# Optimization experiments

Hardware: AMD Instinct MI355X
Metric: run time of the kernel (lower is better)

## Reference

```python
import jax, jax.numpy as jnp
import numpy as np
from math import sqrt

D_MODEL = 768
N_HEADS = 12
D_K = 64
D_V = 64
LN_EPS = 1e-5
NEG = -1e9


def layer_norm(x, g, b):
    mu = jnp.mean(x, axis=-1, keepdims=True)
    var = jnp.mean((x - mu) ** 2, axis=-1, keepdims=True)
    return (x - mu) * jax.lax.rsqrt(var + LN_EPS) * g + b


def setup_inputs() -> dict:
    key = jax.random.key(0)
    ks = jax.random.split(key, 8)
    B, S = 4, 1024
    pro1 = jax.random.normal(ks[0], (B, S, D_MODEL), dtype=jnp.float32)
    pro2 = jax.random.normal(ks[1], (B, S, D_MODEL), dtype=jnp.float32)
    # attn_mask is [B, H, S2, S1]; transpose(2,3) masks scores [B,H,S1,S2]
    mask1_2 = jax.random.bernoulli(ks[2], 0.3, (B, N_HEADS, S, S))
    sc = 1.0 / np.sqrt(D_MODEL)
    W_Q = jax.random.normal(ks[3], (D_MODEL, D_K * N_HEADS), dtype=jnp.float32) * sc
    W_K = jax.random.normal(ks[4], (D_MODEL, D_K * N_HEADS), dtype=jnp.float32) * sc
    fc1 = jax.random.normal(ks[5], (D_V * N_HEADS, D_MODEL), dtype=jnp.float32) * sc
    g1 = jnp.ones((D_MODEL,), jnp.float32)
    b1 = jnp.zeros((D_MODEL,), jnp.float32)
    g2 = jnp.ones((D_MODEL,), jnp.float32)
    b2 = jnp.zeros((D_MODEL,), jnp.float32)
    return {"pro1": pro1, "pro2": pro2, "mask1_2": mask1_2,
            "W_Q": W_Q, "W_K": W_K, "fc1": fc1,
            "g1": g1, "b1": b1, "g2": g2, "b2": b2}


def reference(pro1, pro2, mask1_2, W_Q, W_K, fc1, g1, b1, g2, b2):
    B, S1, _ = pro1.shape
    S2 = pro2.shape[1]
    # project and split heads: [B, H, S, d_k]
    Q = (pro1 @ W_Q).reshape(B, S1, N_HEADS, D_K).transpose(0, 2, 1, 3)
    K = (pro2 @ W_K).reshape(B, S2, N_HEADS, D_K).transpose(0, 2, 1, 3)
    scores = jnp.einsum('bhsd,bhtd->bhst', Q, K) / sqrt(D_K)  # [B,H,S1,S2]
    mask = jnp.swapaxes(mask1_2, 2, 3)  # attn_mask.transpose(2,3)
    scores = jnp.where(mask, NEG, scores)
    attn1 = jax.nn.softmax(scores, axis=-1)                  # over S2
    attn2 = jax.nn.softmax(jnp.swapaxes(scores, -1, -2), axis=-1)  # over S1
    ctx1 = jnp.einsum('bhst,bhtd->bhsd', attn1, K)  # [B,H,S1,d_k]
    ctx2 = jnp.einsum('bhts,bhsd->bhtd', attn2, Q)  # [B,H,S2,d_k]
    c1 = ctx1.transpose(0, 2, 1, 3).reshape(B, S1, N_HEADS * D_V)
    c2 = ctx2.transpose(0, 2, 1, 3).reshape(B, S2, N_HEADS * D_V)
    # NOTE: original applies fc1 to BOTH branches (fc2 is dead code)
    o1 = layer_norm(c1 @ fc1, g1, b1)
    o2 = layer_norm(c2 @ fc1, g2, b2)
    return (o1, o2)
```

## Files before the change

### kernel.cpp

```cpp
#include <hip/hip_runtime.h>
#include <hip/hip_bf16.h>
#include <stdint.h>

#define S 1024
#define DMODEL 768
#define NH 12
#define DK 64
#define BB 4
#define BH 48
#define M4 4096
#define NEGV -1e9f

typedef __attribute__((ext_vector_type(8))) short bf16x8;
typedef __attribute__((ext_vector_type(4))) float f32x4;

static __device__ __forceinline__ unsigned short f2bf(float f) {
  unsigned int u = __float_as_uint(f);
  unsigned int r = u + 0x7FFFu + ((u >> 16) & 1u);
  return (unsigned short)(r >> 16);
}
static __device__ __forceinline__ float bf2f(unsigned short h) {
  return __uint_as_float(((unsigned int)h) << 16);
}
static __device__ __forceinline__ bf16x8 ldfrag(const unsigned short* p) {
  uint4 q = *reinterpret_cast<const uint4*>(p);
  return __builtin_bit_cast(bf16x8, q);
}

__global__ __launch_bounds__(256) void k_convert(const float* __restrict__ in,
                                                 unsigned short* __restrict__ out, int n4) {
  int i = blockIdx.x * 256 + threadIdx.x;
  if (i < n4) {
    float4 v = reinterpret_cast<const float4*>(in)[i];
    ushort4 o;
    o.x = f2bf(v.x); o.y = f2bf(v.y); o.z = f2bf(v.z); o.w = f2bf(v.w);
    reinterpret_cast<ushort4*>(out)[i] = o;
  }
}

__global__ __launch_bounds__(256) void k_transpose(const float* w0, const float* w1, const float* w2,
                                                   unsigned short* o0, unsigned short* o1, unsigned short* o2) {
  const float* in = blockIdx.z == 0 ? w0 : (blockIdx.z == 1 ? w1 : w2);
  unsigned short* out = blockIdx.z == 0 ? o0 : (blockIdx.z == 1 ? o1 : o2);
  __shared__ float tile[32][33];
  int n0 = blockIdx.x * 32, k0 = blockIdx.y * 32;
  int tid = threadIdx.x;
  int r = tid >> 3, c = (tid & 7) * 4;
  float4 v = *reinterpret_cast<const float4*>(in + (size_t)(k0 + r) * DMODEL + n0 + c);
  tile[r][c] = v.x; tile[r][c + 1] = v.y; tile[r][c + 2] = v.z; tile[r][c + 3] = v.w;
  __syncthreads();
  ushort4 o;
  o.x = f2bf(tile[c + 0][r]);
  o.y = f2bf(tile[c + 1][r]);
  o.z = f2bf(tile[c + 2][r]);
  o.w = f2bf(tile[c + 3][r]);
  *reinterpret_cast<ushort4*>(out + (size_t)(n0 + r) * DMODEL + k0 + c) = o;
}

__global__ __launch_bounds__(256) void k_pack(const int* __restrict__ mask,
                                              unsigned int* __restrict__ mp1,
                                              unsigned int* __restrict__ mp2) {
  int bh = blockIdx.y;
  int w = threadIdx.x >> 6, lane = threadIdx.x & 63;
  int tile = blockIdx.x * 4 + w;
  int ti = tile >> 4, tj = tile & 15;
  int t0 = ti * 64, s0 = tj * 64;
  const int* mb = mask + (size_t)bh * S * S;
  unsigned long long rowword = 0;
#pragma unroll 8
  for (int r = 0; r < 64; ++r) {
    int v = mb[(size_t)(t0 + r) * S + s0 + lane];
    unsigned long long b = __ballot(v != 0);
    if (lane == r) rowword = b;
  }
  unsigned int* p2 = mp2 + (size_t)bh * 32 * S;
  p2[((s0 >> 5) + 0) * S + t0 + lane] = (unsigned int)rowword;
  p2[((s0 >> 5) + 1) * S + t0 + lane] = (unsigned int)(rowword >> 32);
  unsigned long long colword = 0;
#pragma unroll
  for (int s = 0; s < 64; ++s) {
    unsigned long long b = __ballot((rowword >> s) & 1ull);
    if (lane == s) colword = b;
  }
  unsigned int* p1 = mp1 + (size_t)bh * 32 * S;
  p1[((t0 >> 5) + 0) * S + s0 + lane] = (unsigned int)colword;
  p1[((t0 >> 5) + 1) * S + s0 + lane] = (unsigned int)(colword >> 32);
}

__global__ __launch_bounds__(256) void k_gemm128(
    int mode,
    const unsigned short* __restrict__ A0, const unsigned short* __restrict__ A1,
    const unsigned short* __restrict__ Bt0, const unsigned short* __restrict__ Bt1,
    unsigned short* __restrict__ oQ0, unsigned short* __restrict__ oQ1,
    unsigned short* __restrict__ oT0, unsigned short* __restrict__ oT1,
    float* __restrict__ oF0, float* __restrict__ oF1) {
  const unsigned short* A = blockIdx.z ? A1 : A0;
  const unsigned short* Bt = blockIdx.z ? Bt1 : Bt0;
  __shared__ __align__(16) unsigned short As[128 * 72];
  __shared__ __align__(16) unsigned short Bs[128 * 72];
  int tid = threadIdx.x;
  int m0 = blockIdx.x * 128, n0 = blockIdx.y * 128;
  int w = tid >> 6, lane = tid & 63, lane15 = lane & 15, quad = lane >> 4;
  int row0 = (w >> 1) * 64, col0 = (w & 1) * 64;
  f32x4 acc[4][4] = {};
  int sr = tid >> 2, sc = (tid & 3) * 16;
  const unsigned short* gA0 = A + (size_t)(m0 + sr) * DMODEL + sc;
  const unsigned short* gA1 = A + (size_t)(m0 + 64 + sr) * DMODEL + sc;
  const unsigned short* gB0 = Bt + (size_t)(n0 + sr) * DMODEL + sc;
  const unsigned short* gB1 = Bt + (size_t)(n0 + 64 + sr) * DMODEL + sc;
  uint4 va0 = *reinterpret_cast<const uint4*>(gA0);
  uint4 va1 = *reinterpret_cast<const uint4*>(gA1);
  uint4 vb0 = *reinterpret_cast<const uint4*>(gB0);
  uint4 vb1 = *reinterpret_cast<const uint4*>(gB1);
  uint4 va0b = *reinterpret_cast<const uint4*>(gA0 + 8);
  uint4 va1b = *reinterpret_cast<const uint4*>(gA1 + 8);
  uint4 vb0b = *reinterpret_cast<const uint4*>(gB0 + 8);
  uint4 vb1b = *reinterpret_cast<const uint4*>(gB1 + 8);
  for (int kc = 0; kc < 12; ++kc) {
    __syncthreads();
    *reinterpret_cast<uint4*>(&As[sr * 72 + sc]) = va0;
    *reinterpret_cast<uint4*>(&As[sr * 72 + sc + 8]) = va0b;
    *reinterpret_cast<uint4*>(&As[(64 + sr) * 72 + sc]) = va1;
    *reinterpret_cast<uint4*>(&As[(64 + sr) * 72 + sc + 8]) = va1b;
    *reinterpret_cast<uint4*>(&Bs[sr * 72 + sc]) = vb0;
    *reinterpret_cast<uint4*>(&Bs[sr * 72 + sc + 8]) = vb0b;
    *reinterpret_cast<uint4*>(&Bs[(64 + sr) * 72 + sc]) = vb1;
    *reinterpret_cast<uint4*>(&Bs[(64 + sr) * 72 + sc + 8]) = vb1b;
    if (kc < 11) {
      int k0 = (kc + 1) * 64;
      va0 = *reinterpret_cast<const uint4*>(gA0 + k0);
      va1 = *reinterpret_cast<const uint4*>(gA1 + k0);
      vb0 = *reinterpret_cast<const uint4*>(gB0 + k0);
      vb1 = *reinterpret_cast<const uint4*>(gB1 + k0);
      va0b = *reinterpret_cast<const uint4*>(gA0 + k0 + 8);
      va1b = *reinterpret_cast<const uint4*>(gA1 + k0 + 8);
      vb0b = *reinterpret_cast<const uint4*>(gB0 + k0 + 8);
      vb1b = *reinterpret_cast<const uint4*>(gB1 + k0 + 8);
    }
    __syncthreads();
#pragma unroll
    for (int ks = 0; ks < 2; ++ks) {
      int kk = ks * 32 + quad * 8;
      bf16x8 a[4], b[4];
#pragma unroll
      for (int i = 0; i < 4; ++i) a[i] = ldfrag(&As[(row0 + i * 16 + lane15) * 72 + kk]);
#pragma unroll
      for (int j = 0; j < 4; ++j) b[j] = ldfrag(&Bs[(col0 + j * 16 + lane15) * 72 + kk]);
#pragma unroll
      for (int i = 0; i < 4; ++i)
#pragma unroll
        for (int j = 0; j < 4; ++j)
          acc[i][j] = __builtin_amdgcn_mfma_f32_16x16x32_bf16(a[i], b[j], acc[i][j], 0, 0, 0);
    }
  }
  if (mode == 0) {
    unsigned short* out = blockIdx.z ? oQ1 : oQ0;
    unsigned short* outT = blockIdx.z ? oT1 : oT0;
#pragma unroll
    for (int i = 0; i < 4; ++i)
#pragma unroll
      for (int j = 0; j < 4; ++j)
#pragma unroll
        for (int reg = 0; reg < 4; ++reg) {
          int m = m0 + row0 + i * 16 + quad * 4 + reg;
          int n = n0 + col0 + j * 16 + lane15;
          int b = m >> 10, s = m & 1023, h = n >> 6, d = n & 63;
          unsigned short bv = f2bf(acc[i][j][reg]);
          out[(((size_t)(b * NH + h)) * S + s) * DK + d] = bv;
          outT[(((size_t)(b * NH + h)) * DK + d) * S + s] = bv;
        }
  } else {
    float* out = blockIdx.z ? oF1 : oF0;
#pragma unroll
    for (int i = 0; i < 4; ++i)
#pragma unroll
      for (int j = 0; j < 4; ++j)
#pragma unroll
        for (int reg = 0; reg < 4; ++reg) {
          int m = m0 + row0 + i * 16 + quad * 4 + reg;
          int n = n0 + col0 + j * 16 + lane15;
          out[(size_t)m * DMODEL + n] = acc[i][j][reg];
        }
  }
}

__global__ __launch_bounds__(256, 4) void k_attn(
    const unsigned short* __restrict__ Qb, const unsigned short* __restrict__ Kb,
    const unsigned short* __restrict__ QT, const unsigned short* __restrict__ KT,
    const unsigned int* __restrict__ mp1, const unsigned int* __restrict__ mp2,
    unsigned short* __restrict__ c1, unsigned short* __restrict__ c2) {
  int bh = blockIdx.y, path = blockIdx.z;
  int s0b = blockIdx.x * 64;
  const unsigned short* X = path ? Kb : Qb;
  const unsigned short* Y = path ? Qb : Kb;
  const unsigned short* YT = path ? QT : KT;
  const unsigned int* mp = path ? mp2 : mp1;
  unsigned short* outc = path ? c2 : c1;

  __shared__ __align__(16) unsigned short YS[64 * 72];
  __shared__ __align__(16) unsigned short YTS[64 * 72];
  __shared__ __align__(16) unsigned short PS[4][16 * 72];
  __shared__ unsigned int MW[64 * 33];

  const unsigned short* Xb = X + (size_t)bh * S * DK;
  const unsigned short* Yb = Y + (size_t)bh * S * DK;
  const unsigned short* YTb = YT + (size_t)bh * DK * S;
  const unsigned int* mb = mp + (size_t)bh * 32 * S;

  int tid = threadIdx.x;
  int w = tid >> 6, lane = tid & 63, lane15 = lane & 15, quad = lane >> 4;
  int s0 = s0b + w * 16;

  {
    int wd = tid >> 3, r8 = (tid & 7) * 8;
    uint4 v0 = *reinterpret_cast<const uint4*>(mb + (size_t)wd * S + s0b + r8);
    uint4 v1 = *reinterpret_cast<const uint4*>(mb + (size_t)wd * S + s0b + r8 + 4);
    MW[(r8 + 0) * 33 + wd] = v0.x; MW[(r8 + 1) * 33 + wd] = v0.y;
    MW[(r8 + 2) * 33 + wd] = v0.z; MW[(r8 + 3) * 33 + wd] = v0.w;
    MW[(r8 + 4) * 33 + wd] = v1.x; MW[(r8 + 5) * 33 + wd] = v1.y;
    MW[(r8 + 6) * 33 + wd] = v1.z; MW[(r8 + 7) * 33 + wd] = v1.w;
  }

  bf16x8 af0 = ldfrag(Xb + (size_t)(s0 + lane15) * DK + quad * 8);
  bf16x8 af1 = ldfrag(Xb + (size_t)(s0 + lane15) * DK + 32 + quad * 8);

  int sr4 = tid >> 2, sc4 = (tid & 3) * 16;
  const unsigned short* gY = Yb + (size_t)sr4 * DK + sc4;
  const unsigned short* gYT = YTb + (size_t)sr4 * S + sc4;
  uint4 y0 = *reinterpret_cast<const uint4*>(gY);
  uint4 y1 = *reinterpret_cast<const uint4*>(gY + 8);
  uint4 t0 = *reinterpret_cast<const uint4*>(gYT);
  uint4 t1 = *reinterpret_cast<const uint4*>(gYT + 8);

  f32x4 outa[4] = {};
  float lsum[4] = {0.f, 0.f, 0.f, 0.f};
  unsigned short* PSw = PS[w];

  for (int jc = 0; jc < 16; ++jc) {
    __syncthreads();
    *reinterpret_cast<uint4*>(&YS[sr4 * 72 + sc4]) = y0;
    *reinterpret_cast<uint4*>(&YS[sr4 * 72 + sc4 + 8]) = y1;
    *reinterpret_cast<uint4*>(&YTS[sr4 * 72 + sc4]) = t0;
    *reinterpret_cast<uint4*>(&YTS[sr4 * 72 + sc4 + 8]) = t1;
    {
      int jn = (jc + 1 < 16) ? (jc + 1) * 64 : jc * 64;
      y0 = *reinterpret_cast<const uint4*>(gY + (size_t)jn * DK);
      y1 = *reinterpret_cast<const uint4*>(gY + (size_t)jn * DK + 8);
      t0 = *reinterpret_cast<const uint4*>(gYT + jn);
      t1 = *reinterpret_cast<const uint4*>(gYT + jn + 8);
    }
    __syncthreads();

    int j0 = jc * 64;
    f32x4 sc[4];
#pragma unroll
    for (int st = 0; st < 4; ++st) {
      bf16x8 b0 = ldfrag(&YS[(st * 16 + lane15) * 72 + quad * 8]);
      bf16x8 b1 = ldfrag(&YS[(st * 16 + lane15) * 72 + 32 + quad * 8]);
      f32x4 a = {};
      a = __builtin_amdgcn_mfma_f32_16x16x32_bf16(af0, b0, a, 0, 0, 0);
      a = __builtin_amdgcn_mfma_f32_16x16x32_bf16(af1, b1, a, 0, 0, 0);
      sc[st] = a;
    }
    int w0 = j0 >> 5;
    unsigned int mw0[4], mw1[4];
#pragma unroll
    for (int reg = 0; reg < 4; ++reg) {
      int r = w * 16 + quad * 4 + reg;
      mw0[reg] = MW[r * 33 + w0];
      mw1[reg] = MW[r * 33 + w0 + 1];
    }
#pragma unroll
    for (int st = 0; st < 4; ++st) {
      unsigned int sh = (unsigned)((st & 1) * 16 + lane15);
#pragma unroll
      for (int reg = 0; reg < 4; ++reg) {
        unsigned int wd = (st < 2) ? mw0[reg] : mw1[reg];
        float e = __expf(sc[st][reg] * 0.125f);
        float p = ((wd >> sh) & 1u) ? 0.f : e;
        lsum[reg] += p;
        PSw[(quad * 4 + reg) * 72 + st * 16 + lane15] = f2bf(p);
      }
    }
#pragma unroll
    for (int half = 0; half < 2; ++half) {
      bf16x8 pa = ldfrag(&PSw[lane15 * 72 + half * 32 + quad * 8]);
#pragma unroll
      for (int dt = 0; dt < 4; ++dt) {
        bf16x8 bb = ldfrag(&YTS[(dt * 16 + lane15) * 72 + half * 32 + quad * 8]);
        outa[dt] = __builtin_amdgcn_mfma_f32_16x16x32_bf16(pa, bb, outa[dt], 0, 0, 0);
      }
    }
  }

#pragma unroll
  for (int reg = 0; reg < 4; ++reg) {
#pragma unroll
    for (int m = 1; m < 16; m <<= 1) lsum[reg] += __shfl_xor(lsum[reg], m);
    lsum[reg] = 1.0f / lsum[reg];
  }
  int b = bh / NH, h = bh % NH;
#pragma unroll
  for (int dt = 0; dt < 4; ++dt)
#pragma unroll
    for (int reg = 0; reg < 4; ++reg) {
      float v = outa[dt][reg] * lsum[reg];
      size_t idx = ((size_t)(b * S) + s0 + quad * 4 + reg) * DMODEL + h * DK + dt * 16 + lane15;
      outc[idx] = f2bf(v);
    }
}

__global__ __launch_bounds__(256) void k_ln(const float* __restrict__ f1, const float* __restrict__ f2,
                                            const float* __restrict__ g1, const float* __restrict__ b1,
                                            const float* __restrict__ g2, const float* __restrict__ b2,
                                            float* __restrict__ out) {
  int rowg = blockIdx.x;
  int sel = rowg >> 12;
  int row = rowg & 4095;
  const float* in = sel ? f2 : f1;
  const float* g = sel ? g2 : g1;
  const float* be = sel ? b2 : b1;
  int tid = threadIdx.x;
  const float* p = in + (size_t)row * DMODEL;
  float x0 = p[tid], x1 = p[tid + 256], x2 = p[tid + 512];
  float s = x0 + x1 + x2;
  float ss = x0 * x0 + x1 * x1 + x2 * x2;
#pragma unroll
  for (int m = 1; m < 64; m <<= 1) { s += __shfl_xor(s, m); ss += __shfl_xor(ss, m); }
  __shared__ float ps[4], pss[4];
  int w = tid >> 6;
  if ((tid & 63) == 0) { ps[w] = s; pss[w] = ss; }
  __syncthreads();
  s = ps[0] + ps[1] + ps[2] + ps[3];
  ss = pss[0] + pss[1] + pss[2] + pss[3];
  float mu = s * (1.0f / 768.0f);
  float var = ss * (1.0f / 768.0f) - mu * mu;
  float rstd = rsqrtf(var + 1e-5f);
  float* o = out + ((size_t)sel * M4 + row) * DMODEL;
  o[tid] = (x0 - mu) * rstd * g[tid] + be[tid];
  o[tid + 256] = (x1 - mu) * rstd * g[tid + 256] + be[tid + 256];
  o[tid + 512] = (x2 - mu) * rstd * g[tid + 512] + be[tid + 512];
}

extern "C" void kernel_launch(void* const* d_in, const int* in_sizes, int n_in,
                              void* d_out, int out_size, void* d_ws, size_t ws_size,
                              hipStream_t stream) {
  const float* pro1 = (const float*)d_in[0];
  const float* pro2 = (const float*)d_in[1];
  const int* mask = (const int*)d_in[2];
  const float* WQ = (const float*)d_in[3];
  const float* WK = (const float*)d_in[4];
  const float* FC1 = (const float*)d_in[5];
  const float* g1 = (const float*)d_in[6];
  const float* b1 = (const float*)d_in[7];
  const float* g2 = (const float*)d_in[8];
  const float* b2 = (const float*)d_in[9];
  float* out = (float*)d_out;
  char* ws = (char*)d_ws;

  unsigned short* pro1b = (unsigned short*)(ws + 0);
  unsigned short* pro2b = (unsigned short*)(ws + 6291456);
  float* f1 = (float*)(ws + 0);
  unsigned short* wqt = (unsigned short*)(ws + 12582912);
  unsigned short* wkt = (unsigned short*)(ws + 13762560);
  unsigned short* fc1t = (unsigned short*)(ws + 14942208);
  unsigned short* Qb = (unsigned short*)(ws + 16121856);
  unsigned short* Kb = (unsigned short*)(ws + 22413312);
  unsigned short* QT = (unsigned short*)(ws + 28704768);
  unsigned short* KT = (unsigned short*)(ws + 34996224);
  unsigned int* mp1 = (unsigned int*)(ws + 41287680);
  unsigned int* mp2 = (unsigned int*)(ws + 47579136);
  float* f2 = (float*)(ws + 41287680);
  unsigned short* c1 = (unsigned short*)(ws + 53870592);
  unsigned short* c2 = (unsigned short*)(ws + 60162048);

  k_convert<<<3072, 256, 0, stream>>>(pro1, pro1b, 786432);
  k_convert<<<3072, 256, 0, stream>>>(pro2, pro2b, 786432);
  k_transpose<<<dim3(24, 24, 3), 256, 0, stream>>>(WQ, WK, FC1, wqt, wkt, fc1t);
  k_pack<<<dim3(64, BH), 256, 0, stream>>>(mask, mp1, mp2);
  k_gemm128<<<dim3(32, 6, 2), 256, 0, stream>>>(0, pro1b, pro2b, wqt, wkt, Qb, Kb, QT, KT, nullptr, nullptr);
  k_attn<<<dim3(16, BH, 2), 256, 0, stream>>>(Qb, Kb, QT, KT, mp1, mp2, c1, c2);
  k_gemm128<<<dim3(32, 6, 2), 256, 0, stream>>>(1, c1, c2, fc1t, fc1t, nullptr, nullptr, nullptr, nullptr, f1, f2);
  k_ln<<<8192, 256, 0, stream>>>(f1, f2, g1, b1, g2, b2, out);
}
```

Before: 442.4 us.

## Fuse input conversion into QK GEMM and keep attention probabilities in registers

The separate fp32-to-bf16 conversion kernels are removed; the projection GEMM now loads fp32 inputs and packs them to bf16 while staging into shared memory. The transposed Q/K copies are written as fp16 using an identity-matrix MFMA to transpose accumulator fragments. The attention kernel processes 128 rows per block (32 per wave). It transposes the probability fragments in registers with an identity fp16 MFMA instead of round-tripping through shared memory, and does the PV product with fp16 MFMAs. This removes the LDS traffic for P and two kernel launches, at the cost of more registers (occupancy hint lowered to 3), extra MFMA work for the transposes, and fp16 precision for P and the transposed operands.

```diff
diff --git a/kernel.cpp b/kernel.cpp
--- a/kernel.cpp
+++ b/kernel.cpp
@@ -9,33 +9,25 @@
 #define BB 4
 #define BH 48
 #define M4 4096
-#define NEGV -1e9f
 
 typedef __attribute__((ext_vector_type(8))) short bf16x8;
 typedef __attribute__((ext_vector_type(4))) float f32x4;
+typedef __attribute__((ext_vector_type(4))) _Float16 f16x4;
 
 static __device__ __forceinline__ unsigned short f2bf(float f) {
   unsigned int u = __float_as_uint(f);
   unsigned int r = u + 0x7FFFu + ((u >> 16) & 1u);
   return (unsigned short)(r >> 16);
 }
-static __device__ __forceinline__ float bf2f(unsigned short h) {
-  return __uint_as_float(((unsigned int)h) << 16);
+static __device__ __forceinline__ unsigned int pk2(float a, float b) {
+  return (unsigned int)f2bf(a) | ((unsigned int)f2bf(b) << 16);
 }
 static __device__ __forceinline__ bf16x8 ldfrag(const unsigned short* p) {
   uint4 q = *reinterpret_cast<const uint4*>(p);
   return __builtin_bit_cast(bf16x8, q);
 }
-
-__global__ __launch_bounds__(256) void k_convert(const float* __restrict__ in,
-                                                 unsigned short* __restrict__ out, int n4) {
-  int i = blockIdx.x * 256 + threadIdx.x;
-  if (i < n4) {
-    float4 v = reinterpret_cast<const float4*>(in)[i];
-    ushort4 o;
-    o.x = f2bf(v.x); o.y = f2bf(v.y); o.z = f2bf(v.z); o.w = f2bf(v.w);
-    reinterpret_cast<ushort4*>(out)[i] = o;
-  }
+static __device__ __forceinline__ unsigned short h2u(_Float16 h) {
+  return __builtin_bit_cast(unsigned short, h);
 }
 
 __global__ __launch_bounds__(256) void k_transpose(const float* w0, const float* w1, const float* w2,
@@ -87,14 +79,16 @@
   p1[((t0 >> 5) + 1) * S + s0 + lane] = (unsigned int)(colword >> 32);
 }
 
-__global__ __launch_bounds__(256) void k_gemm128(
+__global__ __launch_bounds__(256, 2) void k_gemm128(
     int mode,
-    const unsigned short* __restrict__ A0, const unsigned short* __restrict__ A1,
+    const float* __restrict__ Af0, const float* __restrict__ Af1,
+    const unsigned short* __restrict__ Ab0, const unsigned short* __restrict__ Ab1,
     const unsigned short* __restrict__ Bt0, const unsigned short* __restrict__ Bt1,
     unsigned short* __restrict__ oQ0, unsigned short* __restrict__ oQ1,
     unsigned short* __restrict__ oT0, unsigned short* __restrict__ oT1,
     float* __restrict__ oF0, float* __restrict__ oF1) {
-  const unsigned short* A = blockIdx.z ? A1 : A0;
+  const float* Af = blockIdx.z ? Af1 : Af0;
+  const unsigned short* Ab = blockIdx.z ? Ab1 : Ab0;
   const unsigned short* Bt = blockIdx.z ? Bt1 : Bt0;
   __shared__ __align__(16) unsigned short As[128 * 72];
   __shared__ __align__(16) unsigned short Bs[128 * 72];
@@ -104,38 +98,72 @@
   int row0 = (w >> 1) * 64, col0 = (w & 1) * 64;
   f32x4 acc[4][4] = {};
   int sr = tid >> 2, sc = (tid & 3) * 16;
-  const unsigned short* gA0 = A + (size_t)(m0 + sr) * DMODEL + sc;
-  const unsigned short* gA1 = A + (size_t)(m0 + 64 + sr) * DMODEL + sc;
   const unsigned short* gB0 = Bt + (size_t)(n0 + sr) * DMODEL + sc;
   const unsigned short* gB1 = Bt + (size_t)(n0 + 64 + sr) * DMODEL + sc;
-  uint4 va0 = *reinterpret_cast<const uint4*>(gA0);
-  uint4 va1 = *reinterpret_cast<const uint4*>(gA1);
-  uint4 vb0 = *reinterpret_cast<const uint4*>(gB0);
-  uint4 vb1 = *reinterpret_cast<const uint4*>(gB1);
-  uint4 va0b = *reinterpret_cast<const uint4*>(gA0 + 8);
-  uint4 va1b = *reinterpret_cast<const uint4*>(gA1 + 8);
-  uint4 vb0b = *reinterpret_cast<const uint4*>(gB0 + 8);
-  uint4 vb1b = *reinterpret_cast<const uint4*>(gB1 + 8);
+  uint4 vb[2][2];
+  vb[0][0] = *reinterpret_cast<const uint4*>(gB0);
+  vb[0][1] = *reinterpret_cast<const uint4*>(gB0 + 8);
+  vb[1][0] = *reinterpret_cast<const uint4*>(gB1);
+  vb[1][1] = *reinterpret_cast<const uint4*>(gB1 + 8);
+  const float* gAf0 = Af + (size_t)(m0 + sr) * DMODEL + sc;
+  const float* gAf1 = Af + (size_t)(m0 + 64 + sr) * DMODEL + sc;
+  const unsigned short* gAb0 = Ab + (size_t)(m0 + sr) * DMODEL + sc;
+  const unsigned short* gAb1 = Ab + (size_t)(m0 + 64 + sr) * DMODEL + sc;
+  float4 fa[2][4];
+  uint4 va[2][2];
+  if (mode == 0) {
+#pragma unroll
+    for (int g = 0; g < 4; ++g) fa[0][g] = *reinterpret_cast<const float4*>(gAf0 + g * 4);
+#pragma unroll
+    for (int g = 0; g < 4; ++g) fa[1][g] = *reinterpret_cast<const float4*>(gAf1 + g * 4);
+  } else {
+    va[0][0] = *reinterpret_cast<const uint4*>(gAb0);
+    va[0][1] = *reinterpret_cast<const uint4*>(gAb0 + 8);
+    va[1][0] = *reinterpret_cast<const uint4*>(gAb1);
+    va[1][1] = *reinterpret_cast<const uint4*>(gAb1 + 8);
+  }
   for (int kc = 0; kc < 12; ++kc) {
     __syncthreads();
-    *reinterpret_cast<uint4*>(&As[sr * 72 + sc]) = va0;
-    *reinterpret_cast<uint4*>(&As[sr * 72 + sc + 8]) = va0b;
-    *reinterpret_cast<uint4*>(&As[(64 + sr) * 72 + sc]) = va1;
-    *reinterpret_cast<uint4*>(&As[(64 + sr) * 72 + sc + 8]) = va1b;
-    *reinterpret_cast<uint4*>(&Bs[sr * 72 + sc]) = vb0;
-    *reinterpret_cast<uint4*>(&Bs[sr * 72 + sc + 8]) = vb0b;
-    *reinterpret_cast<uint4*>(&Bs[(64 + sr) * 72 + sc]) = vb1;
-    *reinterpret_cast<uint4*>(&Bs[(64 + sr) * 72 + sc + 8]) = vb1b;
+    if (mode == 0) {
+#pragma unroll
+      for (int h2 = 0; h2 < 2; ++h2) {
+        uint4 u0, u1;
+        u0.x = pk2(fa[h2][0].x, fa[h2][0].y); u0.y = pk2(fa[h2][0].z, fa[h2][0].w);
+        u0.z = pk2(fa[h2][1].x, fa[h2][1].y); u0.w = pk2(fa[h2][1].z, fa[h2][1].w);
+        u1.x = pk2(fa[h2][2].x, fa[h2][2].y); u1.y = pk2(fa[h2][2].z, fa[h2][2].w);
+        u1.z = pk2(fa[h2][3].x, fa[h2][3].y); u1.w = pk2(fa[h2][3].z, fa[h2][3].w);
+        *reinterpret_cast<uint4*>(&As[(h2 * 64 + sr) * 72 + sc]) = u0;
+        *reinterpret_cast<uint4*>(&As[(h2 * 64 + sr) * 72 + sc + 8]) = u1;
+      }
+    } else {
+#pragma unroll
+      for (int h2 = 0; h2 < 2; ++h2) {
+        *reinterpret_cast<uint4*>(&As[(h2 * 64 + sr) * 72 + sc]) = va[h2][0];
+        *reinterpret_cast<uint4*>(&As[(h2 * 64 + sr) * 72 + sc + 8]) = va[h2][1];
+      }
+    }
+#pragma unroll
+    for (int h2 = 0; h2 < 2; ++h2) {
+      *reinterpret_cast<uint4*>(&Bs[(h2 * 64 + sr) * 72 + sc]) = vb[h2][0];
+      *reinterpret_cast<uint4*>(&Bs[(h2 * 64 + sr) * 72 + sc + 8]) = vb[h2][1];
+    }
     if (kc < 11) {
       int k0 = (kc + 1) * 64;
-      va0 = *reinterpret_cast<const uint4*>(gA0 + k0);
-      va1 = *reinterpret_cast<const uint4*>(gA1 + k0);
-      vb0 = *reinterpret_cast<const uint4*>(gB0 + k0);
-      vb1 = *reinterpret_cast<const uint4*>(gB1 + k0);
-      va0b = *reinterpret_cast<const uint4*>(gA0 + k0 + 8);
-      va1b = *reinterpret_cast<const uint4*>(gA1 + k0 + 8);
-      vb0b = *reinterpret_cast<const uint4*>(gB0 + k0 + 8);
-      vb1b = *reinterpret_cast<const uint4*>(gB1 + k0 + 8);
+      if (mode == 0) {
+#pragma unroll
+        for (int g = 0; g < 4; ++g) fa[0][g] = *reinterpret_cast<const float4*>(gAf0 + k0 + g * 4);
+#pragma unroll
+        for (int g = 0; g < 4; ++g) fa[1][g] = *reinterpret_cast<const float4*>(gAf1 + k0 + g * 4);
+      } else {
+        va[0][0] = *reinterpret_cast<const uint4*>(gAb0 + k0);
+        va[0][1] = *reinterpret_cast<const uint4*>(gAb0 + k0 + 8);
+        va[1][0] = *reinterpret_cast<const uint4*>(gAb1 + k0);
+        va[1][1] = *reinterpret_cast<const uint4*>(gAb1 + k0 + 8);
+      }
+      vb[0][0] = *reinterpret_cast<const uint4*>(gB0 + k0);
+      vb[0][1] = *reinterpret_cast<const uint4*>(gB0 + k0 + 8);
+      vb[1][0] = *reinterpret_cast<const uint4*>(gB1 + k0);
+      vb[1][1] = *reinterpret_cast<const uint4*>(gB1 + k0 + 8);
     }
     __syncthreads();
 #pragma unroll
@@ -156,19 +184,33 @@
   if (mode == 0) {
     unsigned short* out = blockIdx.z ? oQ1 : oQ0;
     unsigned short* outT = blockIdx.z ? oT1 : oT0;
+    f16x4 iden;
+#pragma unroll
+    for (int i = 0; i < 4; ++i) iden[i] = (_Float16)((quad * 4 + i) == lane15 ? 1.0f : 0.0f);
+    f32x4 zero4 = {};
 #pragma unroll
     for (int i = 0; i < 4; ++i)
 #pragma unroll
-      for (int j = 0; j < 4; ++j)
+      for (int j = 0; j < 4; ++j) {
 #pragma unroll
         for (int reg = 0; reg < 4; ++reg) {
           int m = m0 + row0 + i * 16 + quad * 4 + reg;
           int n = n0 + col0 + j * 16 + lane15;
           int b = m >> 10, s = m & 1023, h = n >> 6, d = n & 63;
-          unsigned short bv = f2bf(acc[i][j][reg]);
-          out[(((size_t)(b * NH + h)) * S + s) * DK + d] = bv;
-          outT[(((size_t)(b * NH + h)) * DK + d) * S + s] = bv;
+          out[(((size_t)(b * NH + h)) * S + s) * DK + d] = f2bf(acc[i][j][reg]);
         }
+        f16x4 cf;
+#pragma unroll
+        for (int reg = 0; reg < 4; ++reg) cf[reg] = (_Float16)acc[i][j][reg];
+        f32x4 tq = __builtin_amdgcn_mfma_f32_16x16x16f16(cf, iden, zero4, 0, 0, 0);
+#pragma unroll
+        for (int reg = 0; reg < 4; ++reg) {
+          int n = n0 + col0 + j * 16 + quad * 4 + reg;
+          int m = m0 + row0 + i * 16 + lane15;
+          int b = m >> 10, s = m & 1023, h = n >> 6, d = n & 63;
+          outT[(((size_t)(b * NH + h)) * DK + d) * S + s] = h2u((_Float16)tq[reg]);
+        }
+      }
   } else {
     float* out = blockIdx.z ? oF1 : oF0;
 #pragma unroll
@@ -184,13 +226,13 @@
   }
 }
 
-__global__ __launch_bounds__(256, 4) void k_attn(
+__global__ __launch_bounds__(256, 3) void k_attn(
     const unsigned short* __restrict__ Qb, const unsigned short* __restrict__ Kb,
     const unsigned short* __restrict__ QT, const unsigned short* __restrict__ KT,
     const unsigned int* __restrict__ mp1, const unsigned int* __restrict__ mp2,
     unsigned short* __restrict__ c1, unsigned short* __restrict__ c2) {
   int bh = blockIdx.y, path = blockIdx.z;
-  int s0b = blockIdx.x * 64;
+  int s0b = blockIdx.x * 128;
   const unsigned short* X = path ? Kb : Qb;
   const unsigned short* Y = path ? Qb : Kb;
   const unsigned short* YT = path ? QT : KT;
@@ -199,8 +241,7 @@
 
   __shared__ __align__(16) unsigned short YS[64 * 72];
   __shared__ __align__(16) unsigned short YTS[64 * 72];
-  __shared__ __align__(16) unsigned short PS[4][16 * 72];
-  __shared__ unsigned int MW[64 * 33];
+  __shared__ unsigned int MW[128 * 33];
 
   const unsigned short* Xb = X + (size_t)bh * S * DK;
   const unsigned short* Yb = Y + (size_t)bh * S * DK;
@@ -209,20 +250,31 @@
 
   int tid = threadIdx.x;
   int w = tid >> 6, lane = tid & 63, lane15 = lane & 15, quad = lane >> 4;
-  int s0 = s0b + w * 16;
+  int s0w = s0b + w * 32;
 
   {
-    int wd = tid >> 3, r8 = (tid & 7) * 8;
-    uint4 v0 = *reinterpret_cast<const uint4*>(mb + (size_t)wd * S + s0b + r8);
-    uint4 v1 = *reinterpret_cast<const uint4*>(mb + (size_t)wd * S + s0b + r8 + 4);
-    MW[(r8 + 0) * 33 + wd] = v0.x; MW[(r8 + 1) * 33 + wd] = v0.y;
-    MW[(r8 + 2) * 33 + wd] = v0.z; MW[(r8 + 3) * 33 + wd] = v0.w;
-    MW[(r8 + 4) * 33 + wd] = v1.x; MW[(r8 + 5) * 33 + wd] = v1.y;
-    MW[(r8 + 6) * 33 + wd] = v1.z; MW[(r8 + 7) * 33 + wd] = v1.w;
-  }
-
-  bf16x8 af0 = ldfrag(Xb + (size_t)(s0 + lane15) * DK + quad * 8);
-  bf16x8 af1 = ldfrag(Xb + (size_t)(s0 + lane15) * DK + 32 + quad * 8);
+    int wd = tid >> 3, rb = (tid & 7) * 16;
+#pragma unroll
+    for (int u = 0; u < 4; ++u) {
+      uint4 v = *reinterpret_cast<const uint4*>(mb + (size_t)wd * S + s0b + rb + u * 4);
+      MW[(rb + u * 4 + 0) * 33 + wd] = v.x;
+      MW[(rb + u * 4 + 1) * 33 + wd] = v.y;
+      MW[(rb + u * 4 + 2) * 33 + wd] = v.z;
+      MW[(rb + u * 4 + 3) * 33 + wd] = v.w;
+    }
+  }
+
+  bf16x8 af[2][2];
+#pragma unroll
+  for (int rg = 0; rg < 2; ++rg) {
+    af[rg][0] = ldfrag(Xb + (size_t)(s0w + rg * 16 + lane15) * DK + quad * 8);
+    af[rg][1] = ldfrag(Xb + (size_t)(s0w + rg * 16 + lane15) * DK + 32 + quad * 8);
+  }
+
+  f16x4 iden;
+#pragma unroll
+  for (int i = 0; i < 4; ++i) iden[i] = (_Float16)((quad * 4 + i) == lane15 ? 1.0f : 0.0f);
+  f32x4 zero4 = {};
 
   int sr4 = tid >> 2, sc4 = (tid & 3) * 16;
   const unsigned short* gY = Yb + (size_t)sr4 * DK + sc4;
@@ -232,9 +284,8 @@
   uint4 t0 = *reinterpret_cast<const uint4*>(gYT);
   uint4 t1 = *reinterpret_cast<const uint4*>(gYT + 8);
 
-  f32x4 outa[4] = {};
-  float lsum[4] = {0.f, 0.f, 0.f, 0.f};
-  unsigned short* PSw = PS[w];
+  f32x4 outa[2][4] = {};
+  float lsum[2][4] = {};
 
   for (int jc = 0; jc < 16; ++jc) {
     __syncthreads();
@@ -252,62 +303,85 @@
     __syncthreads();
 
     int j0 = jc * 64;
-    f32x4 sc[4];
+    int w0 = j0 >> 5;
+    f32x4 sc[2][4];
 #pragma unroll
     for (int st = 0; st < 4; ++st) {
       bf16x8 b0 = ldfrag(&YS[(st * 16 + lane15) * 72 + quad * 8]);
       bf16x8 b1 = ldfrag(&YS[(st * 16 + lane15) * 72 + 32 + quad * 8]);
-      f32x4 a = {};
-      a = __builtin_amdgcn_mfma_f32_16x16x32_bf16(af0, b0, a, 0, 0, 0);
-      a = __builtin_amdgcn_mfma_f32_16x16x32_bf16(af1, b1, a, 0, 0, 0);
-      sc[st] = a;
-    }
-    int w0 = j0 >> 5;
-    unsigned int mw0[4], mw1[4];
+#pragma unroll
+      for (int rg = 0; rg < 2; ++rg) {
+        f32x4 a = {};
+        a = __builtin_amdgcn_mfma_f32_16x16x32_bf16(af[rg][0], b0, a, 0, 0, 0);
+        a = __builtin_amdgcn_mfma_f32_16x16x32_bf16(af[rg][1], b1, a, 0, 0, 0);
+        sc[rg][st] = a;
+      }
+    }
+    f16x4 pfa[2][4];
+#pragma unroll
+    for (int rg = 0; rg < 2; ++rg) {
+      unsigned int mw0[4], mw1[4];
+#pragma unroll
+      for (int reg = 0; reg < 4; ++reg) {
+        int r = w * 32 + rg * 16 + quad * 4 + reg;
+        mw0[reg] = MW[r * 33 + w0];
+        mw1[reg] = MW[r * 33 + w0 + 1];
+      }
+#pragma unroll
+      for (int st = 0; st < 4; ++st) {
+        unsigned int sh = (unsigned)((st & 1) * 16 + lane15);
+#pragma unroll
+        for (int reg = 0; reg < 4; ++reg) {
+          unsigned int wd = (st < 2) ? mw0[reg] : mw1[reg];
+          float e = __expf(sc[rg][st][reg] * 0.125f);
+          float p = ((wd >> sh) & 1u) ? 0.f : e;
+          lsum[rg][reg] += p;
+          pfa[rg][st][reg] = (_Float16)p;
+        }
+      }
+    }
+#pragma unroll
+    for (int st = 0; st < 4; ++st) {
+      f16x4 ptb[2];
+#pragma unroll
+      for (int rg = 0; rg < 2; ++rg) {
+        f32x4 pt = __builtin_amdgcn_mfma_f32_16x16x16f16(pfa[rg][st], iden, zero4, 0, 0, 0);
+        f16x4 pb;
+#pragma unroll
+        for (int i = 0; i < 4; ++i) pb[i] = (_Float16)pt[i];
+        ptb[rg] = pb;
+      }
+#pragma unroll
+      for (int dt = 0; dt < 4; ++dt) {
+        uint2 q = *reinterpret_cast<const uint2*>(&YTS[(dt * 16 + lane15) * 72 + st * 16 + quad * 4]);
+        f16x4 yb = __builtin_bit_cast(f16x4, q);
+#pragma unroll
+        for (int rg = 0; rg < 2; ++rg)
+          outa[rg][dt] = __builtin_amdgcn_mfma_f32_16x16x16f16(ptb[rg], yb, outa[rg][dt], 0, 0, 0);
+      }
+    }
+  }
+
+#pragma unroll
+  for (int rg = 0; rg < 2; ++rg)
 #pragma unroll
     for (int reg = 0; reg < 4; ++reg) {
-      int r = w * 16 + quad * 4 + reg;
-      mw0[reg] = MW[r * 33 + w0];
-      mw1[reg] = MW[r * 33 + w0 + 1];
-    }
-#pragma unroll
-    for (int st = 0; st < 4; ++st) {
-      unsigned int sh = (unsigned)((st & 1) * 16 + lane15);
+#pragma unroll
+      for (int m = 1; m < 16; m <<= 1) lsum[rg][reg] += __shfl_xor(lsum[rg][reg], m);
+      lsum[rg][reg] = 1.0f / lsum[rg][reg];
+    }
+  int b = bh / NH, h = bh % NH;
+#pragma unroll
+  for (int rg = 0; rg < 2; ++rg)
+#pragma unroll
+    for (int dt = 0; dt < 4; ++dt)
 #pragma unroll
       for (int reg = 0; reg < 4; ++reg) {
-        unsigned int wd = (st < 2) ? mw0[reg] : mw1[reg];
-        float e = __expf(sc[st][reg] * 0.125f);
-        float p = ((wd >> sh) & 1u) ? 0.f : e;
-        lsum[reg] += p;
-        PSw[(quad * 4 + reg) * 72 + st * 16 + lane15] = f2bf(p);
-      }
-    }
-#pragma unroll
-    for (int half = 0; half < 2; ++half) {
-      bf16x8 pa = ldfrag(&PSw[lane15 * 72 + half * 32 + quad * 8]);
-#pragma unroll
-      for (int dt = 0; dt < 4; ++dt) {
-        bf16x8 bb = ldfrag(&YTS[(dt * 16 + lane15) * 72 + half * 32 + quad * 8]);
-        outa[dt] = __builtin_amdgcn_mfma_f32_16x16x32_bf16(pa, bb, outa[dt], 0, 0, 0);
-      }
-    }
-  }
-
-#pragma unroll
-  for (int reg = 0; reg < 4; ++reg) {
-#pragma unroll
-    for (int m = 1; m < 16; m <<= 1) lsum[reg] += __shfl_xor(lsum[reg], m);
-    lsum[reg] = 1.0f / lsum[reg];
-  }
-  int b = bh / NH, h = bh % NH;
-#pragma unroll
-  for (int dt = 0; dt < 4; ++dt)
-#pragma unroll
-    for (int reg = 0; reg < 4; ++reg) {
-      float v = outa[dt][reg] * lsum[reg];
-      size_t idx = ((size_t)(b * S) + s0 + quad * 4 + reg) * DMODEL + h * DK + dt * 16 + lane15;
-      outc[idx] = f2bf(v);
-    }
+        float v = outa[rg][dt][reg] * lsum[rg][reg];
+        int srow = s0w + rg * 16 + quad * 4 + reg;
+        size_t idx = ((size_t)(b * S) + srow) * DMODEL + h * DK + dt * 16 + lane15;
+        outc[idx] = f2bf(v);
+      }
 }
 
 __global__ __launch_bounds__(256) void k_ln(const float* __restrict__ f1, const float* __restrict__ f2,
@@ -358,8 +432,6 @@
   float* out = (float*)d_out;
   char* ws = (char*)d_ws;
 
-  unsigned short* pro1b = (unsigned short*)(ws + 0);
-  unsigned short* pro2b = (unsigned short*)(ws + 6291456);
   float* f1 = (float*)(ws + 0);
   unsigned short* wqt = (unsigned short*)(ws + 12582912);
   unsigned short* wkt = (unsigned short*)(ws + 13762560);
@@ -374,12 +446,12 @@
   unsigned short* c1 = (unsigned short*)(ws + 53870592);
   unsigned short* c2 = (unsigned short*)(ws + 60162048);
 
-  k_convert<<<3072, 256, 0, stream>>>(pro1, pro1b, 786432);
-  k_convert<<<3072, 256, 0, stream>>>(pro2, pro2b, 786432);
   k_transpose<<<dim3(24, 24, 3), 256, 0, stream>>>(WQ, WK, FC1, wqt, wkt, fc1t);
   k_pack<<<dim3(64, BH), 256, 0, stream>>>(mask, mp1, mp2);
-  k_gemm128<<<dim3(32, 6, 2), 256, 0, stream>>>(0, pro1b, pro2b, wqt, wkt, Qb, Kb, QT, KT, nullptr, nullptr);
-  k_attn<<<dim3(16, BH, 2), 256, 0, stream>>>(Qb, Kb, QT, KT, mp1, mp2, c1, c2);
-  k_gemm128<<<dim3(32, 6, 2), 256, 0, stream>>>(1, c1, c2, fc1t, fc1t, nullptr, nullptr, nullptr, nullptr, f1, f2);
+  k_gemm128<<<dim3(32, 6, 2), 256, 0, stream>>>(0, pro1, pro2, nullptr, nullptr, wqt, wkt,
+                                                Qb, Kb, QT, KT, nullptr, nullptr);
+  k_attn<<<dim3(8, BH, 2), 256, 0, stream>>>(Qb, Kb, QT, KT, mp1, mp2, c1, c2);
+  k_gemm128<<<dim3(32, 6, 2), 256, 0, stream>>>(1, nullptr, nullptr, c1, c2, fc1t, fc1t,
+                                                nullptr, nullptr, nullptr, nullptr, f1, f2);
   k_ln<<<8192, 256, 0, stream>>>(f1, f2, g1, b1, g2, b2, out);
 }
```

Result: slower. 480.0 us (+8.5%).
